# Kernel tuning notes

Hardware: AMD Instinct MI355X
Metric: run time of the kernel (lower is better)

## Reference

```python
import jax, jax.numpy as jnp
import numpy as np

B, N, R, CIN = 2, 2048, 128, 256
RADIUS, NSAMPLE, OUT = 0.3, 16, 5
EPS = 1e-5


def setup_inputs():
    key = jax.random.key(0)
    ks = jax.random.split(key, 8)
    points_xyz = jax.random.uniform(ks[0], (B, N, 3)) * 2.0          # scene ~2m cube
    features = jax.random.normal(ks[1], (B, CIN, N))
    ctr = jax.random.uniform(ks[2], (B, R, 3)) * 2.0
    size = jax.random.uniform(ks[3], (B, R, 3)) * 0.6 + 0.3          # positive box sizes
    ang = jax.random.uniform(ks[4], (B, R, 1)) * np.pi
    rois = jnp.concatenate([ctr, size, ang], axis=-1)                # [B,R,7]
    s = 0.02
    W_mlp = jax.random.normal(ks[5], (256, CIN + 3)) * s
    g_mlp = jnp.ones((256,)); bt_mlp = jnp.zeros((256,))
    W1 = jax.random.normal(ks[6], (128, 256)) * s; b1 = jnp.zeros((128,))
    g1 = jnp.ones((128,)); bt1 = jnp.zeros((128,))
    W2 = jax.random.normal(ks[7], (128, 128)) * s; b2 = jnp.zeros((128,))
    g2 = jnp.ones((128,)); bt2 = jnp.zeros((128,))
    return dict(points_xyz=points_xyz, features=features, rois=rois,
                W_mlp=W_mlp, g_mlp=g_mlp, bt_mlp=bt_mlp,
                W1=W1, b1=b1, g1=g1, bt1=bt1,
                W2=W2, b2=b2, g2=g2, bt2=bt2)


def _bn(x, g, b, axes, shape):
    # training-mode BatchNorm (batch statistics), matching torch .train() forward
    m = jnp.mean(x, axes, keepdims=True)
    v = jnp.var(x, axes, keepdims=True)
    return (x - m) * jax.lax.rsqrt(v + EPS) * g.reshape(shape) + b.reshape(shape)


def _forward(points_xyz, features, rois, W_mlp, g_mlp, bt_mlp,
             W1, b1, g1, bt1, W2, b2, g2, bt2):
    # ---- QueryAndGroup: ball query (min_radius=0) + gather + center + normalize_xyz ----
    diff = points_xyz[:, :, None, :] - points_xyz[:, None, :, :]     # [B,Nq,Np,3]
    d2 = jnp.sum(diff * diff, -1)
    mask = d2 < RADIUS * RADIUS
    cand = jnp.where(mask, jnp.arange(N, dtype=jnp.int32)[None, None, :], N)
    idx = jnp.sort(cand, axis=-1)[..., :NSAMPLE]                     # first NSAMPLE in-ball, ascending point index
    idx = jnp.where(idx < N, idx, idx[..., :1])                      # pad with first valid (self always in-ball)
    gx = jax.vmap(lambda p, i: p[i])(points_xyz, idx)                # [B,N,S,3]
    gx = (gx - points_xyz[:, :, None, :]) / RADIUS                   # centered + normalized
    gf = jax.vmap(lambda f, i: f[i])(jnp.swapaxes(features, 1, 2), idx)  # [B,N,S,C]
    nf = jnp.transpose(jnp.concatenate([gx, gf], -1), (0, 3, 1, 2))  # [B,3+C,N,S] (use_xyz=True)
    # ---- mlp: Conv2d 1x1 (bias='auto' with BN -> no bias) + BN2d + ReLU ----
    h = jnp.einsum('oc,bcns->bons', W_mlp, nf)
    h = jax.nn.relu(_bn(h, g_mlp, bt_mlp, (0, 2, 3), (1, -1, 1, 1)))
    feats = jnp.max(h, -1)                                           # max_pool2d over samples -> [B,256,N]
    h = jnp.einsum('oc,bcn->bon', W1, feats) + b1[None, :, None]
    h = jax.nn.relu(_bn(h, g1, bt1, (0, 2), (1, -1, 1)))
    h = jnp.einsum('oc,bcn->bon', W2, h) + b2[None, :, None]
    feats = jax.nn.relu(_bn(h, g2, bt2, (0, 2), (1, -1, 1)))         # [B,128,N]
    # ---- RoIPool3d: roi-aware voxel max pool (out_size=5, mode='max') ----
    C = feats.shape[1]
    ctr, size, ry = rois[..., :3], rois[..., 3:6], rois[..., 6]
    rel = points_xyz[:, None, :, :] - ctr[:, :, None, :]             # [B,R,N,3]
    c = jnp.cos(ry)[:, :, None]; s = jnp.sin(ry)[:, :, None]
    lx = rel[..., 0] * c + rel[..., 1] * s                           # rotate by -ry into roi frame
    ly = -rel[..., 0] * s + rel[..., 1] * c
    local = jnp.stack([lx, ly, rel[..., 2]], -1)                     # [B,R,N,3]
    half = size[:, :, None, :] * 0.5
    inside = jnp.all(jnp.abs(local) < half, -1)                      # [B,R,N]
    v = jnp.clip(jnp.floor((local + half) / (2.0 * half) * OUT), 0, OUT - 1).astype(jnp.int32)
    vox = (v[..., 0] * OUT + v[..., 1]) * OUT + v[..., 2]
    base = jnp.arange(B * R, dtype=jnp.int32).reshape(B, R, 1) * (OUT ** 3)
    seg = jnp.where(inside, base + vox, B * R * OUT ** 3).reshape(-1)  # dummy segment for outside pts
    data = jnp.broadcast_to(jnp.swapaxes(feats, 1, 2)[:, None], (B, R, N, C)).reshape(-1, C)
    pooled = jax.ops.segment_max(data, seg, num_segments=B * R * OUT ** 3 + 1)[:-1]
    pooled = jnp.where(jnp.isneginf(pooled), 0.0, pooled)            # empty voxels -> 0
    roi_feats = pooled.reshape(B, R, OUT, OUT, OUT, C)
    return feats, roi_feats


def reference(points_xyz, features, rois, W_mlp, g_mlp, bt_mlp,
              W1, b1, g1, bt1, W2, b2, g2, bt2):
    return _forward(points_xyz, features, rois, W_mlp, g_mlp, bt_mlp,
                    W1, b1, g1, bt1, W2, b2, g2, bt2)
```

## Files before the change

kernel.cpp:

```cpp
#include <hip/hip_runtime.h>
#include <hip/hip_bf16.h>

typedef __hip_bfloat16 bf16;
typedef unsigned short u16;

#define NB   2
#define NPT  2048
#define NROI 128
#define CINF 256
#define NS   16
#define KDIM 259
#define KP2  288
#define C1   256
#define C2   128
#define NVOX 125
#define EPSF 1e-5f

typedef __bf16 bf16x8 __attribute__((ext_vector_type(8)));
typedef float  f32x4  __attribute__((ext_vector_type(4)));

__device__ __forceinline__ float ldin(const void* p, size_t i, int f32flag) {
    if (f32flag) return ((const float*)p)[i];
    unsigned short u = ((const unsigned short*)p)[i];
    return __uint_as_float(((unsigned)u) << 16);
}

__device__ __forceinline__ unsigned short f2bf(float x) {
    unsigned u = __float_as_uint(x);
    u += 0x7FFFu + ((u >> 16) & 1u);
    return (unsigned short)(u >> 16);
}


__global__ void k_detect(const void* __restrict__ Wm, int* __restrict__ flag) {
    __shared__ int f;
    int tid = threadIdx.x;
    if (tid == 0) f = 0;
    __syncthreads();
    #pragma unroll
    for (int r = 0; r < 4; r++) {
        unsigned short u = ((const unsigned short*)Wm)[r * 256 + tid];
        float v = __uint_as_float(((unsigned)u) << 16);
        if (!(fabsf(v) <= 1e4f)) atomicOr(&f, 1);
    }
    __syncthreads();
    if (tid == 0) *flag = f;
}

__global__ void k_cvt(const void* __restrict__ pts, const void* __restrict__ rois,
                      const void* __restrict__ gm, const void* __restrict__ btm,
                      const void* __restrict__ b1, const void* __restrict__ g1,
                      const void* __restrict__ bt1, const void* __restrict__ b2,
                      const void* __restrict__ g2, const void* __restrict__ bt2,
                      const void* __restrict__ Wm,
                      float* __restrict__ ptsf, float* __restrict__ roisf,
                      float* __restrict__ params, const int* __restrict__ flag) {
    int f = *flag;
    int e = blockIdx.x * 256 + threadIdx.x;
    if (blockIdx.y == 10) {
        if (e < 768) {
            int d = e >> 8, o = e & 255;
            params[25088 + e] = ldin(Wm, (size_t)o * KDIM + d, f);
        }
        return;
    }
    const void* src; float* dst; int n;
    switch (blockIdx.y) {
        case 0:  src = pts; dst = ptsf;           n = NB * NPT * 3; break;
        case 1:  src = rois; dst = roisf;         n = NB * NROI * 7; break;
        case 2:  src = gm;  dst = params + 0;     n = 256; break;
        case 3:  src = btm; dst = params + 256;   n = 256; break;
        case 4:  src = b1;  dst = params + 33280; n = 128; break;
        case 5:  src = g1;  dst = params + 33408; n = 128; break;
        case 6:  src = bt1; dst = params + 33536; n = 128; break;
        case 7:  src = b2;  dst = params + 50048; n = 128; break;
        case 8:  src = g2;  dst = params + 50176; n = 128; break;
        default: src = bt2; dst = params + 50304; n = 128; break;
    }
    if (e < n) dst[e] = ldin(src, e, f);
}

__global__ void k_soa(const float* __restrict__ ptsf, float* __restrict__ psx,
                      float* __restrict__ psy, float* __restrict__ psz) {
    int e = blockIdx.x * 256 + threadIdx.x;
    if (e < NB * NPT) {
        psx[e] = ptsf[e * 3 + 0];
        psy[e] = ptsf[e * 3 + 1];
        psz[e] = ptsf[e * 3 + 2];
    }
}

__global__ void k_transpose(const void* __restrict__ feat, u16* __restrict__ ftbf,
                            const int* __restrict__ flag) {
    __shared__ float tile[32][33];
    int f = *flag;
    int b = blockIdx.z;
    int n0 = blockIdx.x * 32, c0 = blockIdx.y * 32;
    int tx = threadIdx.x, ty = threadIdx.y;
    #pragma unroll
    for (int d = 0; d < 4; d++) {
        int c = c0 + ty + d * 8;
        tile[ty + d * 8][tx] = ldin(feat, ((size_t)(b * CINF + c)) * NPT + n0 + tx, f);
    }
    __syncthreads();
    #pragma unroll
    for (int d = 0; d < 4; d++) {
        int n = n0 + ty + d * 8;
        ftbf[((size_t)(b * NPT + n)) * CINF + c0 + tx] = f2bf(tile[tx][ty + d * 8]);
    }
}

__global__ void k_prep(const void* __restrict__ Wm, const void* __restrict__ W1,
                       const void* __restrict__ W2, u16* __restrict__ wbf,
                       u16* __restrict__ w1bf, u16* __restrict__ w2bf,
                       float* __restrict__ stats, const int* __restrict__ flag) {
    int f = *flag;
    int e = blockIdx.x * 256 + threadIdx.x;
    if (e < 256 * KP2) {
        int o = e / KP2, k = e % KP2;
        float v = 0.f;
        if (k < 256)      v = ldin(Wm, (size_t)o * KDIM + 3 + k, f);
        else if (k < 259) v = ldin(Wm, (size_t)o * KDIM + (k - 256), f);
        wbf[e] = f2bf(v);
    } else if (e < 256 * KP2 + 1024) {
        stats[e - 256 * KP2] = 0.f;
    } else if (e < 256 * KP2 + 1024 + 32768) {
        int idx = e - (256 * KP2 + 1024);
        w1bf[idx] = f2bf(ldin(W1, idx, f));
    } else if (e < 256 * KP2 + 1024 + 32768 + 16384) {
        int idx = e - (256 * KP2 + 1024 + 32768);
        w2bf[idx] = f2bf(ldin(W2, idx, f));
    }
}

__global__ __launch_bounds__(256) void k_knn2(const float* __restrict__ psx, const float* __restrict__ psy,
                                              const float* __restrict__ psz, int* __restrict__ idxb) {
    #pragma clang fp contract(off)
    int wid = threadIdx.x >> 6, lane = threadIdx.x & 63;
    int q = blockIdx.x * 4 + wid;
    int b = q >> 11;
    int base = b * NPT;
    float qx = psx[q], qy = psy[q], qz = psz[q];
    const float R2 = (float)(0.3 * 0.3);
    size_t ob = (size_t)q * NS;
    int cnt = 0, j0 = -1;
    unsigned long long below = (lane == 63) ? ~0ull >> 1 : ((1ull << (lane + 1)) - 1) >> 1;
    for (int c0 = 0; c0 < NPT; c0 += 64) {
        int j = c0 + lane;
        float dx = qx - psx[base + j];
        float dy = qy - psy[base + j];
        float dz = qz - psz[base + j];
        float d2 = dx * dx + dy * dy + dz * dz;
        bool hit = d2 < R2;
        unsigned long long m = __ballot(hit);
        if (m) {
            if (j0 < 0) j0 = c0 + __builtin_ctzll(m);
            int pos = cnt + __popcll(m & below);
            if (hit && pos < NS) idxb[ob + pos] = j;
            cnt += __popcll(m);
        }
        if (cnt >= NS) break;
    }
    if (lane >= cnt && lane < NS) idxb[ob + lane] = j0;
}

__global__ __launch_bounds__(256) void k_dense(const u16* __restrict__ ftbf, const u16* __restrict__ wbf,
                                               float* __restrict__ Hf) {
    int w = threadIdx.x >> 6, lane = threadIdx.x & 63;
    int lg = lane >> 4, lr = lane & 15;
    int rbase = blockIdx.x * 16;
    int c0 = blockIdx.y * 128 + w * 32;

    size_t aoff  = (size_t)(rbase + lr) * CINF + lg * 8;
    size_t boff0 = (size_t)(c0 + lr) * KP2 + lg * 8;
    size_t boff1 = (size_t)(c0 + 16 + lr) * KP2 + lg * 8;

    f32x4 acc0 = (f32x4){0.f, 0.f, 0.f, 0.f};
    f32x4 acc1 = (f32x4){0.f, 0.f, 0.f, 0.f};
    #pragma unroll
    for (int k0 = 0; k0 < 256; k0 += 32) {
        bf16x8 af = __builtin_bit_cast(bf16x8, *(const uint4*)(ftbf + aoff + k0));
        bf16x8 b0 = __builtin_bit_cast(bf16x8, *(const uint4*)(wbf + boff0 + k0));
        bf16x8 b1 = __builtin_bit_cast(bf16x8, *(const uint4*)(wbf + boff1 + k0));
        acc0 = __builtin_amdgcn_mfma_f32_16x16x32_bf16(af, b0, acc0, 0, 0, 0);
        acc1 = __builtin_amdgcn_mfma_f32_16x16x32_bf16(af, b1, acc1, 0, 0, 0);
    }
    #pragma unroll
    for (int r = 0; r < 4; r++) {
        int row = rbase + lg * 4 + r;
        Hf[(size_t)row * C1 + c0 + lr] = acc0[r];
        Hf[(size_t)row * C1 + c0 + 16 + lr] = acc1[r];
    }
}

#define GPTS 8
__global__ __launch_bounds__(256) void k_gather(const float* __restrict__ Hf, const int* __restrict__ idxb,
                                                const float* __restrict__ ptsf, const float* __restrict__ wxyz,
                                                float* __restrict__ Hmax, float* __restrict__ Hmin,
                                                float* __restrict__ stats) {
    __shared__ int   lj[NS];
    __shared__ float lgx[NS], lgy[NS], lgz[NS];
    int o = threadIdx.x;
    float wx = wxyz[o], wy = wxyz[256 + o], wz = wxyz[512 + o];
    float ssum = 0.f, ssq = 0.f;
    for (int p = 0; p < GPTS; p++) {
        int pt = blockIdx.x * GPTS + p;
        int b = pt >> 11;
        int base = b * NPT;
        if (o < NS) {
            int j = idxb[(size_t)pt * NS + o];
            lj[o] = j;
            size_t jb = ((size_t)(base + j)) * 3;
            size_t cb = (size_t)pt * 3;
            lgx[o] = (ptsf[jb]     - ptsf[cb])     / 0.3f;
            lgy[o] = (ptsf[jb + 1] - ptsf[cb + 1]) / 0.3f;
            lgz[o] = (ptsf[jb + 2] - ptsf[cb + 2]) / 0.3f;
        }
        __syncthreads();
        float mx = -3.4e38f, mn = 3.4e38f;
        #pragma unroll
        for (int s = 0; s < NS; s++) {
            float v = Hf[(size_t)(base + lj[s]) * C1 + o] + wx * lgx[s] + wy * lgy[s] + wz * lgz[s];
            mx = fmaxf(mx, v); mn = fminf(mn, v);
            ssum += v; ssq += v * v;
        }
        Hmax[(size_t)pt * C1 + o] = mx;
        Hmin[(size_t)pt * C1 + o] = mn;
        __syncthreads();
    }
    atomicAdd(&stats[o], ssum);
    atomicAdd(&stats[256 + o], ssq);
}

__global__ void k_feats0(const float* __restrict__ Hmax, const float* __restrict__ Hmin,
                         const float* __restrict__ stats, const float* __restrict__ g,
                         const float* __restrict__ bt, u16* __restrict__ f0bf) {
    int e = blockIdx.x * 256 + threadIdx.x;
    if (e >= NB * NPT * C1) return;
    int o = e & (C1 - 1);
    const float inv = 1.f / 65536.f;
    float m = stats[o] * inv;
    float var = fmaxf(stats[256 + o] * inv - m * m, 0.f);
    float a = g[o] / sqrtf(var + EPSF);
    float d = bt[o] - m * a;
    float h = (a > 0.f) ? Hmax[e] : Hmin[e];
    f0bf[e] = f2bf(fmaxf(a * h + d, 0.f));
}

template<int K>
__global__ __launch_bounds__(256) void k_lin(const u16* __restrict__ Xbf, const u16* __restrict__ Wb,
                                             const float* __restrict__ bias, float* __restrict__ out,
                                             float* __restrict__ sum, float* __restrict__ sumsq) {
    int w = threadIdx.x >> 6, lane = threadIdx.x & 63;
    int lg = lane >> 4, lr = lane & 15;
    int rbase = blockIdx.x * 16;
    int c0 = w * 32;

    size_t aoff = (size_t)(rbase + lr) * K + lg * 8;
    size_t boff0 = (size_t)(c0 + lr) * K + lg * 8;
    size_t boff1 = (size_t)(c0 + 16 + lr) * K + lg * 8;

    f32x4 acc0 = (f32x4){0.f, 0.f, 0.f, 0.f};
    f32x4 acc1 = (f32x4){0.f, 0.f, 0.f, 0.f};
    #pragma unroll
    for (int k0 = 0; k0 < K; k0 += 32) {
        bf16x8 af = __builtin_bit_cast(bf16x8, *(const uint4*)(Xbf + aoff + k0));
        bf16x8 b0 = __builtin_bit_cast(bf16x8, *(const uint4*)(Wb + boff0 + k0));
        bf16x8 b1 = __builtin_bit_cast(bf16x8, *(const uint4*)(Wb + boff1 + k0));
        acc0 = __builtin_amdgcn_mfma_f32_16x16x32_bf16(af, b0, acc0, 0, 0, 0);
        acc1 = __builtin_amdgcn_mfma_f32_16x16x32_bf16(af, b1, acc1, 0, 0, 0);
    }

    #pragma unroll
    for (int ct = 0; ct < 2; ct++) {
        f32x4 a = ct ? acc1 : acc0;
        int col = c0 + ct * 16 + lr;
        float bi = bias[col];
        float s = 0.f, q = 0.f;
        #pragma unroll
        for (int r = 0; r < 4; r++) {
            float h = a[r] + bi;
            out[(size_t)(rbase + lg * 4 + r) * C2 + col] = h;
            s += h; q += h * h;
        }
        s += __shfl_xor(s, 16); s += __shfl_xor(s, 32);
        q += __shfl_xor(q, 16); q += __shfl_xor(q, 32);
        if (lane < 16) {
            atomicAdd(&sum[col], s);
            atomicAdd(&sumsq[col], q);
        }
    }
}

__global__ void k_bnrelu(const float* __restrict__ h, const float* __restrict__ sum,
                         const float* __restrict__ sumsq, const float* __restrict__ g,
                         const float* __restrict__ bt, u16* __restrict__ xbf) {
    int e = blockIdx.x * 256 + threadIdx.x;
    if (e >= NB * NPT * C2) return;
    int o = e & (C2 - 1);
    const float inv = 1.f / 4096.f;
    float m = sum[o] * inv;
    float var = fmaxf(sumsq[o] * inv - m * m, 0.f);
    float a = g[o] / sqrtf(var + EPSF);
    float d = bt[o] - m * a;
    xbf[e] = f2bf(fmaxf(a * h[e] + d, 0.f));
}

__global__ void k_final(const float* __restrict__ h2, const float* __restrict__ sum,
                        const float* __restrict__ sumsq, const float* __restrict__ g,
                        const float* __restrict__ bt, float* __restrict__ fp,
                        void* __restrict__ out0, const int* __restrict__ flag) {
    int e = blockIdx.x * 256 + threadIdx.x;
    if (e >= NB * NPT * C2) return;
    int f = *flag;
    int o = e & (C2 - 1);
    int bn = e >> 7;
    int b = bn >> 11, n = bn & (NPT - 1);
    const float inv = 1.f / 4096.f;
    float m = sum[o] * inv;
    float var = fmaxf(sumsq[o] * inv - m * m, 0.f);
    float a = g[o] / sqrtf(var + EPSF);
    float d = bt[o] - m * a;
    float v = fmaxf(a * h2[e] + d, 0.f);
    fp[e] = v;
    size_t oi = ((size_t)(b * C2 + o)) * NPT + n;
    if (f) ((float*)out0)[oi] = v;
    else   ((unsigned short*)out0)[oi] = f2bf(v);
}

__global__ __launch_bounds__(512) void k_pool2(const float* __restrict__ ptsf, const float* __restrict__ roisf,
                                               const float* __restrict__ fp, void* __restrict__ d_out,
                                               const int* __restrict__ flag, int* __restrict__ glist) {
    #pragma clang fp contract(off)
    __shared__ int pooled[NVOX * C2];
    __shared__ int cnt;
    __shared__ float rp[8];
    int f = *flag;
    int bid = blockIdx.x;
    int b = bid >> 7;
    int tid = threadIdx.x;
    for (int k = tid; k < NVOX * C2; k += 512) pooled[k] = 0;
    if (tid == 0) {
        cnt = 0;
        size_t rb = ((size_t)bid) * 7;
        rp[0] = roisf[rb];     rp[1] = roisf[rb + 1]; rp[2] = roisf[rb + 2];
        rp[3] = roisf[rb + 3] * 0.5f;
        rp[4] = roisf[rb + 4] * 0.5f;
        rp[5] = roisf[rb + 5] * 0.5f;
        float ry = roisf[rb + 6];
        rp[6] = (float)cos((double)ry);
        rp[7] = (float)sin((double)ry);
    }
    __syncthreads();
    float cx = rp[0], cy = rp[1], cz = rp[2];
    float hx = rp[3], hy = rp[4], hz = rp[5];
    float cf = rp[6], sf = rp[7];
    int* mylist = glist + bid * NPT;
    for (int n = tid; n < NPT; n += 512) {
        size_t pb = ((size_t)(b * NPT + n)) * 3;
        float rx  = ptsf[pb]     - cx;
        float ryy = ptsf[pb + 1] - cy;
        float rz  = ptsf[pb + 2] - cz;
        float lx = rx * cf + ryy * sf;
        float ly = -rx * sf + ryy * cf;
        if (fabsf(lx) < hx && fabsf(ly) < hy && fabsf(rz) < hz) {
            int vx = (int)fminf(fmaxf(floorf((lx + hx) / (2.f * hx) * 5.f), 0.f), 4.f);
            int vy = (int)fminf(fmaxf(floorf((ly + hy) / (2.f * hy) * 5.f), 0.f), 4.f);
            int vz = (int)fminf(fmaxf(floorf((rz + hz) / (2.f * hz) * 5.f), 0.f), 4.f);
            int vox = (vx * 5 + vy) * 5 + vz;
            int pos = atomicAdd(&cnt, 1);
            mylist[pos] = (vox << 16) | n;
        }
    }
    __syncthreads();
    int m = cnt;
    int c = tid & 127, slot = tid >> 7;
    for (int e = slot; e < m; e += 4) {
        int u = mylist[e];
        int n = u & 0xFFFF, vox = u >> 16;
        float v = fp[((size_t)(b * NPT + n)) * C2 + c];
        atomicMax(&pooled[vox * C2 + c], __float_as_int(v));
    }
    __syncthreads();
    size_t ob = (size_t)524288 + (size_t)bid * (NVOX * C2);
    for (int k = tid; k < NVOX * C2; k += 512) {
        float v = __int_as_float(pooled[k]);
        if (f) ((float*)d_out)[ob + k] = v;
        else   ((unsigned short*)d_out)[ob + k] = f2bf(v);
    }
}

extern "C" void kernel_launch(void* const* d_in, const int* in_sizes, int n_in,
                              void* d_out, int out_size, void* d_ws, size_t ws_size,
                              hipStream_t stream) {
    const void* pts  = d_in[0];
    const void* feat = d_in[1];
    const void* rois = d_in[2];
    const void* Wm   = d_in[3];
    const void* gm   = d_in[4];
    const void* btm  = d_in[5];
    const void* W1   = d_in[6];
    const void* b1   = d_in[7];
    const void* g1   = d_in[8];
    const void* bt1  = d_in[9];
    const void* W2   = d_in[10];
    const void* b2   = d_in[11];
    const void* g2   = d_in[12];
    const void* bt2  = d_in[13];

    float* ws     = (float*)d_ws;
    int*   flag   = (int*)ws;
    float* ptsf   = ws + 16;
    float* roisf  = ws + 12304;
    float* params = ws + 14096;
    u16*   w1bf   = (u16*)(params + 512);
    u16*   w2bf   = (u16*)(params + 512 + 16384);
    float* wxyz   = params + 25088;
    u16*   wbf    = (u16*)(ws + 64528);
    float* stats  = ws + 101392;
    int*   idxb   = (int*)(ws + 102416);
    u16*   ftbf   = (u16*)(ws + 167952);
    float* Hmax   = ws + 1216528;
    float* Hmin   = ws + 2265104;
    u16*   f0bf   = (u16*)(ws + 167952);
    float* h1     = ws + 1216528;
    u16*   x1bf   = (u16*)(ws + 1740816);
    float* h2     = ws + 2265104;
    float* fp     = ws + 2789392;
    float* psx    = ws + 3313680;
    float* psy    = ws + 3317776;
    float* psz    = ws + 3321872;
    float* Hf     = ws + 3325968;
    int*   glist  = (int*)(ws + 3325968);

    k_detect<<<1, 256, 0, stream>>>(Wm, flag);
    k_cvt<<<dim3(48, 11), 256, 0, stream>>>(pts, rois, gm, btm, b1, g1, bt1, b2, g2, bt2, Wm,
                                            ptsf, roisf, params, flag);
    k_soa<<<16, 256, 0, stream>>>(ptsf, psx, psy, psz);
    k_transpose<<<dim3(NPT / 32, CINF / 32, NB), dim3(32, 8), 0, stream>>>(feat, ftbf, flag);
    k_prep<<<484, 256, 0, stream>>>(Wm, W1, W2, wbf, w1bf, w2bf, stats, flag);
    k_knn2<<<NB * NPT / 4, 256, 0, stream>>>(psx, psy, psz, idxb);
    k_dense<<<dim3(256, 2), 256, 0, stream>>>(ftbf, wbf, Hf);
    k_gather<<<(NB * NPT) / GPTS, 256, 0, stream>>>(Hf, idxb, ptsf, wxyz, Hmax, Hmin, stats);
    k_feats0<<<(NB * NPT * C1) / 256, 256, 0, stream>>>(Hmax, Hmin, stats, params + 0, params + 256, f0bf);
    k_lin<256><<<256, 256, 0, stream>>>(f0bf, w1bf, params + 33280, h1, stats + 512, stats + 640);
    k_bnrelu<<<(NB * NPT * C2) / 256, 256, 0, stream>>>(h1, stats + 512, stats + 640, params + 33408, params + 33536, x1bf);
    k_lin<128><<<256, 256, 0, stream>>>(x1bf, w2bf, params + 50048, h2, stats + 768, stats + 896);
    k_final<<<(NB * NPT * C2) / 256, 256, 0, stream>>>(h2, stats + 768, stats + 896, params + 50176, params + 50304, fp, d_out, flag);
    k_pool2<<<NB * NROI, 512, 0, stream>>>(ptsf, roisf, fp, d_out, flag, glist);
}
```

Measured before the change: 196.1 us.

## Merge setup kernels, co-launch ball query with dense GEMM, fuse BN-ReLU into linears

Folds the dtype-detect, convert, SoA, transpose and weight-prep kernels into one block-indexed setup kernel, with each block recomputing the dtype flag from the first weights. Ball query and the dense feature GEMM now share one launch as disjoint block ranges. The BatchNorm+ReLU stages are fused into the prologues of the two following linear kernels, which build bf16 activation tiles in shared memory. Together these cut the launch count from fourteen to seven and drop two intermediate bf16 buffers, at the cost of redundant flag reads in every block and a more heterogeneous setup kernel.

```diff
diff --git a/kernel.cpp b/kernel.cpp
--- a/kernel.cpp
+++ b/kernel.cpp
@@ -31,165 +31,165 @@
     return (unsigned short)(u >> 16);
 }
 
-
-__global__ void k_detect(const void* __restrict__ Wm, int* __restrict__ flag) {
-    __shared__ int f;
+__device__ __forceinline__ int detect_flag(const void* __restrict__ Wm) {
+    const uint4* p = (const uint4*)Wm;
+    int bad = 0;
+    #pragma unroll
+    for (int i = 0; i < 8; i++) {
+        uint4 v = p[i];
+        unsigned w[4] = {v.x, v.y, v.z, v.w};
+        #pragma unroll
+        for (int j = 0; j < 4; j++) {
+            if (!(fabsf(__uint_as_float(w[j] << 16)) <= 1e4f)) bad = 1;
+            if (!(fabsf(__uint_as_float(w[j] & 0xFFFF0000u)) <= 1e4f)) bad = 1;
+        }
+    }
+    return bad;
+}
+
+
+__global__ __launch_bounds__(256) void k_setup(
+    const void* __restrict__ pts, const void* __restrict__ feat, const void* __restrict__ rois,
+    const void* __restrict__ Wm, const void* __restrict__ gm, const void* __restrict__ btm,
+    const void* __restrict__ W1, const void* __restrict__ b1, const void* __restrict__ g1,
+    const void* __restrict__ bt1, const void* __restrict__ W2, const void* __restrict__ b2,
+    const void* __restrict__ g2, const void* __restrict__ bt2,
+    float* __restrict__ ptsf, float* __restrict__ roisf, float* __restrict__ params,
+    u16* __restrict__ wbf, u16* __restrict__ w1bf, u16* __restrict__ w2bf,
+    float* __restrict__ stats, u16* __restrict__ ftbf,
+    float* __restrict__ psx, float* __restrict__ psy, float* __restrict__ psz) {
+    int f = detect_flag(Wm);
+    int bx = blockIdx.x;
     int tid = threadIdx.x;
-    if (tid == 0) f = 0;
-    __syncthreads();
-    #pragma unroll
-    for (int r = 0; r < 4; r++) {
-        unsigned short u = ((const unsigned short*)Wm)[r * 256 + tid];
-        float v = __uint_as_float(((unsigned)u) << 16);
-        if (!(fabsf(v) <= 1e4f)) atomicOr(&f, 1);
-    }
-    __syncthreads();
-    if (tid == 0) *flag = f;
-}
-
-__global__ void k_cvt(const void* __restrict__ pts, const void* __restrict__ rois,
-                      const void* __restrict__ gm, const void* __restrict__ btm,
-                      const void* __restrict__ b1, const void* __restrict__ g1,
-                      const void* __restrict__ bt1, const void* __restrict__ b2,
-                      const void* __restrict__ g2, const void* __restrict__ bt2,
-                      const void* __restrict__ Wm,
-                      float* __restrict__ ptsf, float* __restrict__ roisf,
-                      float* __restrict__ params, const int* __restrict__ flag) {
-    int f = *flag;
-    int e = blockIdx.x * 256 + threadIdx.x;
-    if (blockIdx.y == 10) {
-        if (e < 768) {
-            int d = e >> 8, o = e & 255;
-            params[25088 + e] = ldin(Wm, (size_t)o * KDIM + d, f);
-        }
-        return;
-    }
-    const void* src; float* dst; int n;
-    switch (blockIdx.y) {
-        case 0:  src = pts; dst = ptsf;           n = NB * NPT * 3; break;
-        case 1:  src = rois; dst = roisf;         n = NB * NROI * 7; break;
-        case 2:  src = gm;  dst = params + 0;     n = 256; break;
-        case 3:  src = btm; dst = params + 256;   n = 256; break;
-        case 4:  src = b1;  dst = params + 33280; n = 128; break;
-        case 5:  src = g1;  dst = params + 33408; n = 128; break;
-        case 6:  src = bt1; dst = params + 33536; n = 128; break;
-        case 7:  src = b2;  dst = params + 50048; n = 128; break;
-        case 8:  src = g2;  dst = params + 50176; n = 128; break;
-        default: src = bt2; dst = params + 50304; n = 128; break;
-    }
-    if (e < n) dst[e] = ldin(src, e, f);
-}
-
-__global__ void k_soa(const float* __restrict__ ptsf, float* __restrict__ psx,
-                      float* __restrict__ psy, float* __restrict__ psz) {
-    int e = blockIdx.x * 256 + threadIdx.x;
-    if (e < NB * NPT) {
-        psx[e] = ptsf[e * 3 + 0];
-        psy[e] = ptsf[e * 3 + 1];
-        psz[e] = ptsf[e * 3 + 2];
-    }
-}
-
-__global__ void k_transpose(const void* __restrict__ feat, u16* __restrict__ ftbf,
-                            const int* __restrict__ flag) {
-    __shared__ float tile[32][33];
-    int f = *flag;
-    int b = blockIdx.z;
-    int n0 = blockIdx.x * 32, c0 = blockIdx.y * 32;
-    int tx = threadIdx.x, ty = threadIdx.y;
-    #pragma unroll
-    for (int d = 0; d < 4; d++) {
-        int c = c0 + ty + d * 8;
-        tile[ty + d * 8][tx] = ldin(feat, ((size_t)(b * CINF + c)) * NPT + n0 + tx, f);
-    }
-    __syncthreads();
-    #pragma unroll
-    for (int d = 0; d < 4; d++) {
-        int n = n0 + ty + d * 8;
-        ftbf[((size_t)(b * NPT + n)) * CINF + c0 + tx] = f2bf(tile[tx][ty + d * 8]);
-    }
-}
-
-__global__ void k_prep(const void* __restrict__ Wm, const void* __restrict__ W1,
-                       const void* __restrict__ W2, u16* __restrict__ wbf,
-                       u16* __restrict__ w1bf, u16* __restrict__ w2bf,
-                       float* __restrict__ stats, const int* __restrict__ flag) {
-    int f = *flag;
-    int e = blockIdx.x * 256 + threadIdx.x;
-    if (e < 256 * KP2) {
+    if (bx < 1024) {
+        __shared__ float tile[32][33];
+        int b = bx >> 9;
+        int r = bx & 511;
+        int n0 = (r & 63) * 32, c0 = (r >> 6) * 32;
+        int tx = tid & 31, ty = tid >> 5;
+        #pragma unroll
+        for (int d = 0; d < 4; d++) {
+            int c = c0 + ty + d * 8;
+            tile[ty + d * 8][tx] = ldin(feat, ((size_t)(b * CINF + c)) * NPT + n0 + tx, f);
+        }
+        __syncthreads();
+        #pragma unroll
+        for (int d = 0; d < 4; d++) {
+            int n = n0 + ty + d * 8;
+            ftbf[((size_t)(b * NPT + n)) * CINF + c0 + tx] = f2bf(tile[tx][ty + d * 8]);
+        }
+    } else if (bx < 1312) {
+        int e = (bx - 1024) * 256 + tid;
         int o = e / KP2, k = e % KP2;
         float v = 0.f;
         if (k < 256)      v = ldin(Wm, (size_t)o * KDIM + 3 + k, f);
         else if (k < 259) v = ldin(Wm, (size_t)o * KDIM + (k - 256), f);
         wbf[e] = f2bf(v);
-    } else if (e < 256 * KP2 + 1024) {
-        stats[e - 256 * KP2] = 0.f;
-    } else if (e < 256 * KP2 + 1024 + 32768) {
-        int idx = e - (256 * KP2 + 1024);
-        w1bf[idx] = f2bf(ldin(W1, idx, f));
-    } else if (e < 256 * KP2 + 1024 + 32768 + 16384) {
-        int idx = e - (256 * KP2 + 1024 + 32768);
-        w2bf[idx] = f2bf(ldin(W2, idx, f));
-    }
-}
-
-__global__ __launch_bounds__(256) void k_knn2(const float* __restrict__ psx, const float* __restrict__ psy,
-                                              const float* __restrict__ psz, int* __restrict__ idxb) {
-    #pragma clang fp contract(off)
-    int wid = threadIdx.x >> 6, lane = threadIdx.x & 63;
-    int q = blockIdx.x * 4 + wid;
-    int b = q >> 11;
-    int base = b * NPT;
-    float qx = psx[q], qy = psy[q], qz = psz[q];
-    const float R2 = (float)(0.3 * 0.3);
-    size_t ob = (size_t)q * NS;
-    int cnt = 0, j0 = -1;
-    unsigned long long below = (lane == 63) ? ~0ull >> 1 : ((1ull << (lane + 1)) - 1) >> 1;
-    for (int c0 = 0; c0 < NPT; c0 += 64) {
-        int j = c0 + lane;
-        float dx = qx - psx[base + j];
-        float dy = qy - psy[base + j];
-        float dz = qz - psz[base + j];
-        float d2 = dx * dx + dy * dy + dz * dz;
-        bool hit = d2 < R2;
-        unsigned long long m = __ballot(hit);
-        if (m) {
-            if (j0 < 0) j0 = c0 + __builtin_ctzll(m);
-            int pos = cnt + __popcll(m & below);
-            if (hit && pos < NS) idxb[ob + pos] = j;
-            cnt += __popcll(m);
-        }
-        if (cnt >= NS) break;
-    }
-    if (lane >= cnt && lane < NS) idxb[ob + lane] = j0;
-}
-
-__global__ __launch_bounds__(256) void k_dense(const u16* __restrict__ ftbf, const u16* __restrict__ wbf,
-                                               float* __restrict__ Hf) {
-    int w = threadIdx.x >> 6, lane = threadIdx.x & 63;
-    int lg = lane >> 4, lr = lane & 15;
-    int rbase = blockIdx.x * 16;
-    int c0 = blockIdx.y * 128 + w * 32;
-
-    size_t aoff  = (size_t)(rbase + lr) * CINF + lg * 8;
-    size_t boff0 = (size_t)(c0 + lr) * KP2 + lg * 8;
-    size_t boff1 = (size_t)(c0 + 16 + lr) * KP2 + lg * 8;
-
-    f32x4 acc0 = (f32x4){0.f, 0.f, 0.f, 0.f};
-    f32x4 acc1 = (f32x4){0.f, 0.f, 0.f, 0.f};
-    #pragma unroll
-    for (int k0 = 0; k0 < 256; k0 += 32) {
-        bf16x8 af = __builtin_bit_cast(bf16x8, *(const uint4*)(ftbf + aoff + k0));
-        bf16x8 b0 = __builtin_bit_cast(bf16x8, *(const uint4*)(wbf + boff0 + k0));
-        bf16x8 b1 = __builtin_bit_cast(bf16x8, *(const uint4*)(wbf + boff1 + k0));
-        acc0 = __builtin_amdgcn_mfma_f32_16x16x32_bf16(af, b0, acc0, 0, 0, 0);
-        acc1 = __builtin_amdgcn_mfma_f32_16x16x32_bf16(af, b1, acc1, 0, 0, 0);
-    }
-    #pragma unroll
-    for (int r = 0; r < 4; r++) {
-        int row = rbase + lg * 4 + r;
-        Hf[(size_t)row * C1 + c0 + lr] = acc0[r];
-        Hf[(size_t)row * C1 + c0 + 16 + lr] = acc1[r];
+    } else if (bx < 1440) {
+        int e = (bx - 1312) * 256 + tid;
+        w1bf[e] = f2bf(ldin(W1, e, f));
+    } else if (bx < 1504) {
+        int e = (bx - 1440) * 256 + tid;
+        w2bf[e] = f2bf(ldin(W2, e, f));
+    } else if (bx < 1552) {
+        int e = (bx - 1504) * 256 + tid;
+        if (e < NB * NPT * 3) ptsf[e] = ldin(pts, e, f);
+    } else if (bx < 1559) {
+        int e = (bx - 1552) * 256 + tid;
+        if (e < NB * NROI * 7) roisf[e] = ldin(rois, e, f);
+    } else if (bx < 1567) {
+        int t = bx - 1559;
+        const void* src; int off, n;
+        switch (t) {
+            case 0: src = gm;  off = 0;     n = 256; break;
+            case 1: src = btm; off = 256;   n = 256; break;
+            case 2: src = b1;  off = 33280; n = 128; break;
+            case 3: src = g1;  off = 33408; n = 128; break;
+            case 4: src = bt1; off = 33536; n = 128; break;
+            case 5: src = b2;  off = 50048; n = 128; break;
+            case 6: src = g2;  off = 50176; n = 128; break;
+            default: src = bt2; off = 50304; n = 128; break;
+        }
+        if (tid < n) params[off + tid] = ldin(src, tid, f);
+    } else if (bx < 1570) {
+        int e = (bx - 1567) * 256 + tid;
+        if (e < 768) {
+            int d = e >> 8, o = e & 255;
+            params[25088 + e] = ldin(Wm, (size_t)o * KDIM + d, f);
+        }
+    } else if (bx < 1586) {
+        int e = (bx - 1570) * 256 + tid;
+        if (e < NB * NPT) {
+            psx[e] = ptsf ? ldin(pts, e * 3 + 0, f) : 0.f;
+            psy[e] = ldin(pts, e * 3 + 1, f);
+            psz[e] = ldin(pts, e * 3 + 2, f);
+        }
+    } else {
+        int e = (bx - 1586) * 256 + tid;
+        if (e < 1024) stats[e] = 0.f;
+    }
+}
+
+__global__ __launch_bounds__(256) void k_qd(const float* __restrict__ psx, const float* __restrict__ psy,
+                                            const float* __restrict__ psz, int* __restrict__ idxb,
+                                            const u16* __restrict__ ftbf, const u16* __restrict__ wbf,
+                                            float* __restrict__ Hf) {
+    int bx = blockIdx.x;
+    if (bx < 1024) {
+        #pragma clang fp contract(off)
+        int wid = threadIdx.x >> 6, lane = threadIdx.x & 63;
+        int q = bx * 4 + wid;
+        int b = q >> 11;
+        int base = b * NPT;
+        float qx = psx[q], qy = psy[q], qz = psz[q];
+        const float R2 = (float)(0.3 * 0.3);
+        size_t ob = (size_t)q * NS;
+        int cnt = 0, j0 = -1;
+        unsigned long long below = (lane == 63) ? ~0ull >> 1 : ((1ull << (lane + 1)) - 1) >> 1;
+        for (int c0 = 0; c0 < NPT; c0 += 64) {
+            int j = c0 + lane;
+            float dx = qx - psx[base + j];
+            float dy = qy - psy[base + j];
+            float dz = qz - psz[base + j];
+            float d2 = dx * dx + dy * dy + dz * dz;
+            bool hit = d2 < R2;
+            unsigned long long m = __ballot(hit);
+            if (m) {
+                if (j0 < 0) j0 = c0 + __builtin_ctzll(m);
+                int pos = cnt + __popcll(m & below);
+                if (hit && pos < NS) idxb[ob + pos] = j;
+                cnt += __popcll(m);
+            }
+            if (cnt >= NS) break;
+        }
+        if (lane >= cnt && lane < NS) idxb[ob + lane] = j0;
+    } else {
+        int bx2 = bx - 1024;
+        int w = threadIdx.x >> 6, lane = threadIdx.x & 63;
+        int lg = lane >> 4, lr = lane & 15;
+        int rbase = (bx2 & 255) * 16;
+        int c0 = (bx2 >> 8) * 128 + w * 32;
+
+        size_t aoff  = (size_t)(rbase + lr) * CINF + lg * 8;
+        size_t boff0 = (size_t)(c0 + lr) * KP2 + lg * 8;
+        size_t boff1 = (size_t)(c0 + 16 + lr) * KP2 + lg * 8;
+
+        f32x4 acc0 = (f32x4){0.f, 0.f, 0.f, 0.f};
+        f32x4 acc1 = (f32x4){0.f, 0.f, 0.f, 0.f};
+        #pragma unroll
+        for (int k0 = 0; k0 < 256; k0 += 32) {
+            bf16x8 af = __builtin_bit_cast(bf16x8, *(const uint4*)(ftbf + aoff + k0));
+            bf16x8 b0 = __builtin_bit_cast(bf16x8, *(const uint4*)(wbf + boff0 + k0));
+            bf16x8 b1 = __builtin_bit_cast(bf16x8, *(const uint4*)(wbf + boff1 + k0));
+            acc0 = __builtin_amdgcn_mfma_f32_16x16x32_bf16(af, b0, acc0, 0, 0, 0);
+            acc1 = __builtin_amdgcn_mfma_f32_16x16x32_bf16(af, b1, acc1, 0, 0, 0);
+        }
+        #pragma unroll
+        for (int r = 0; r < 4; r++) {
+            int row = rbase + lg * 4 + r;
+            Hf[(size_t)row * C1 + c0 + lr] = acc0[r];
+            Hf[(size_t)row * C1 + c0 + 16 + lr] = acc1[r];
+        }
     }
 }
 
@@ -232,45 +232,45 @@
     atomicAdd(&stats[256 + o], ssq);
 }
 
-__global__ void k_feats0(const float* __restrict__ Hmax, const float* __restrict__ Hmin,
-                         const float* __restrict__ stats, const float* __restrict__ g,
-                         const float* __restrict__ bt, u16* __restrict__ f0bf) {
-    int e = blockIdx.x * 256 + threadIdx.x;
-    if (e >= NB * NPT * C1) return;
-    int o = e & (C1 - 1);
-    const float inv = 1.f / 65536.f;
-    float m = stats[o] * inv;
-    float var = fmaxf(stats[256 + o] * inv - m * m, 0.f);
-    float a = g[o] / sqrtf(var + EPSF);
-    float d = bt[o] - m * a;
-    float h = (a > 0.f) ? Hmax[e] : Hmin[e];
-    f0bf[e] = f2bf(fmaxf(a * h + d, 0.f));
-}
-
-template<int K>
-__global__ __launch_bounds__(256) void k_lin(const u16* __restrict__ Xbf, const u16* __restrict__ Wb,
-                                             const float* __restrict__ bias, float* __restrict__ out,
-                                             float* __restrict__ sum, float* __restrict__ sumsq) {
-    int w = threadIdx.x >> 6, lane = threadIdx.x & 63;
+__global__ __launch_bounds__(256) void k_lin1f(const float* __restrict__ Hmax, const float* __restrict__ Hmin,
+                                               const float* __restrict__ stats, const float* __restrict__ g,
+                                               const float* __restrict__ bt, const u16* __restrict__ Wb,
+                                               const float* __restrict__ bias, float* __restrict__ out,
+                                               float* __restrict__ sum, float* __restrict__ sumsq) {
+    __shared__ __align__(16) u16 xa[16][264];
+    int tid = threadIdx.x;
+    int rbase = blockIdx.x * 16;
+    {
+        int c = tid;
+        const float inv = 1.f / 65536.f;
+        float m = stats[c] * inv;
+        float var = fmaxf(stats[256 + c] * inv - m * m, 0.f);
+        float a = g[c] / sqrtf(var + EPSF);
+        float d = bt[c] - m * a;
+        #pragma unroll
+        for (int r = 0; r < 16; r++) {
+            size_t e = (size_t)(rbase + r) * C1 + c;
+            float h = (a > 0.f) ? Hmax[e] : Hmin[e];
+            xa[r][c] = f2bf(fmaxf(a * h + d, 0.f));
+        }
+    }
+    __syncthreads();
+    int w = tid >> 6, lane = tid & 63;
     int lg = lane >> 4, lr = lane & 15;
-    int rbase = blockIdx.x * 16;
     int c0 = w * 32;
-
-    size_t aoff = (size_t)(rbase + lr) * K + lg * 8;
-    size_t boff0 = (size_t)(c0 + lr) * K + lg * 8;
-    size_t boff1 = (size_t)(c0 + 16 + lr) * K + lg * 8;
+    size_t boff0 = (size_t)(c0 + lr) * 256 + lg * 8;
+    size_t boff1 = (size_t)(c0 + 16 + lr) * 256 + lg * 8;
 
     f32x4 acc0 = (f32x4){0.f, 0.f, 0.f, 0.f};
     f32x4 acc1 = (f32x4){0.f, 0.f, 0.f, 0.f};
     #pragma unroll
-    for (int k0 = 0; k0 < K; k0 += 32) {
-        bf16x8 af = __builtin_bit_cast(bf16x8, *(const uint4*)(Xbf + aoff + k0));
+    for (int k0 = 0; k0 < 256; k0 += 32) {
+        bf16x8 af = __builtin_bit_cast(bf16x8, *(const uint4*)&xa[lr][k0 + lg * 8]);
         bf16x8 b0 = __builtin_bit_cast(bf16x8, *(const uint4*)(Wb + boff0 + k0));
         bf16x8 b1 = __builtin_bit_cast(bf16x8, *(const uint4*)(Wb + boff1 + k0));
         acc0 = __builtin_amdgcn_mfma_f32_16x16x32_bf16(af, b0, acc0, 0, 0, 0);
         acc1 = __builtin_amdgcn_mfma_f32_16x16x32_bf16(af, b1, acc1, 0, 0, 0);
     }
-
     #pragma unroll
     for (int ct = 0; ct < 2; ct++) {
         f32x4 a = ct ? acc1 : acc0;
@@ -292,27 +292,73 @@
     }
 }
 
-__global__ void k_bnrelu(const float* __restrict__ h, const float* __restrict__ sum,
-                         const float* __restrict__ sumsq, const float* __restrict__ g,
-                         const float* __restrict__ bt, u16* __restrict__ xbf) {
-    int e = blockIdx.x * 256 + threadIdx.x;
-    if (e >= NB * NPT * C2) return;
-    int o = e & (C2 - 1);
-    const float inv = 1.f / 4096.f;
-    float m = sum[o] * inv;
-    float var = fmaxf(sumsq[o] * inv - m * m, 0.f);
-    float a = g[o] / sqrtf(var + EPSF);
-    float d = bt[o] - m * a;
-    xbf[e] = f2bf(fmaxf(a * h[e] + d, 0.f));
+__global__ __launch_bounds__(256) void k_lin2f(const float* __restrict__ h1, const float* __restrict__ stats1,
+                                               const float* __restrict__ g, const float* __restrict__ bt,
+                                               const u16* __restrict__ Wb, const float* __restrict__ bias,
+                                               float* __restrict__ out, float* __restrict__ sum,
+                                               float* __restrict__ sumsq) {
+    __shared__ __align__(16) u16 xa[16][136];
+    int tid = threadIdx.x;
+    int rbase = blockIdx.x * 16;
+    {
+        int c = tid & 127, half = tid >> 7;
+        const float inv = 1.f / 4096.f;
+        float m = stats1[c] * inv;
+        float var = fmaxf(stats1[128 + c] * inv - m * m, 0.f);
+        float a = g[c] / sqrtf(var + EPSF);
+        float d = bt[c] - m * a;
+        #pragma unroll
+        for (int rr = 0; rr < 8; rr++) {
+            int r = half * 8 + rr;
+            float h = h1[(size_t)(rbase + r) * C2 + c];
+            xa[r][c] = f2bf(fmaxf(a * h + d, 0.f));
+        }
+    }
+    __syncthreads();
+    int w = tid >> 6, lane = tid & 63;
+    int lg = lane >> 4, lr = lane & 15;
+    int c0 = w * 32;
+    size_t boff0 = (size_t)(c0 + lr) * 128 + lg * 8;
+    size_t boff1 = (size_t)(c0 + 16 + lr) * 128 + lg * 8;
+
+    f32x4 acc0 = (f32x4){0.f, 0.f, 0.f, 0.f};
+    f32x4 acc1 = (f32x4){0.f, 0.f, 0.f, 0.f};
+    #pragma unroll
+    for (int k0 = 0; k0 < 128; k0 += 32) {
+        bf16x8 af = __builtin_bit_cast(bf16x8, *(const uint4*)&xa[lr][k0 + lg * 8]);
+        bf16x8 b0 = __builtin_bit_cast(bf16x8, *(const uint4*)(Wb + boff0 + k0));
+        bf16x8 b1 = __builtin_bit_cast(bf16x8, *(const uint4*)(Wb + boff1 + k0));
+        acc0 = __builtin_amdgcn_mfma_f32_16x16x32_bf16(af, b0, acc0, 0, 0, 0);
+        acc1 = __builtin_amdgcn_mfma_f32_16x16x32_bf16(af, b1, acc1, 0, 0, 0);
+    }
+    #pragma unroll
+    for (int ct = 0; ct < 2; ct++) {
+        f32x4 a = ct ? acc1 : acc0;
+        int col = c0 + ct * 16 + lr;
+        float bi = bias[col];
+        float s = 0.f, q = 0.f;
+        #pragma unroll
+        for (int r = 0; r < 4; r++) {
+            float h = a[r] + bi;
+            out[(size_t)(rbase + lg * 4 + r) * C2 + col] = h;
+            s += h; q += h * h;
+        }
+        s += __shfl_xor(s, 16); s += __shfl_xor(s, 32);
+        q += __shfl_xor(q, 16); q += __shfl_xor(q, 32);
+        if (lane < 16) {
+            atomicAdd(&sum[col], s);
+            atomicAdd(&sumsq[col], q);
+        }
+    }
 }
 
 __global__ void k_final(const float* __restrict__ h2, const float* __restrict__ sum,
                         const float* __restrict__ sumsq, const float* __restrict__ g,
                         const float* __restrict__ bt, float* __restrict__ fp,
-                        void* __restrict__ out0, const int* __restrict__ flag) {
+                        void* __restrict__ out0, const void* __restrict__ Wm) {
     int e = blockIdx.x * 256 + threadIdx.x;
     if (e >= NB * NPT * C2) return;
-    int f = *flag;
+    int f = detect_flag(Wm);
     int o = e & (C2 - 1);
     int bn = e >> 7;
     int b = bn >> 11, n = bn & (NPT - 1);
@@ -330,12 +376,12 @@
 
 __global__ __launch_bounds__(512) void k_pool2(const float* __restrict__ ptsf, const float* __restrict__ roisf,
                                                const float* __restrict__ fp, void* __restrict__ d_out,
-                                               const int* __restrict__ flag, int* __restrict__ glist) {
+                                               const void* __restrict__ Wm, int* __restrict__ glist) {
     #pragma clang fp contract(off)
     __shared__ int pooled[NVOX * C2];
     __shared__ int cnt;
     __shared__ float rp[8];
-    int f = *flag;
+    int f = detect_flag(Wm);
     int bid = blockIdx.x;
     int b = bid >> 7;
     int tid = threadIdx.x;
@@ -409,7 +455,6 @@
     const void* bt2  = d_in[13];
 
     float* ws     = (float*)d_ws;
-    int*   flag   = (int*)ws;
     float* ptsf   = ws + 16;
     float* roisf  = ws + 12304;
     float* params = ws + 14096;
@@ -422,9 +467,7 @@
     u16*   ftbf   = (u16*)(ws + 167952);
     float* Hmax   = ws + 1216528;
     float* Hmin   = ws + 2265104;
-    u16*   f0bf   = (u16*)(ws + 167952);
     float* h1     = ws + 1216528;
-    u16*   x1bf   = (u16*)(ws + 1740816);
     float* h2     = ws + 2265104;
     float* fp     = ws + 2789392;
     float* psx    = ws + 3313680;
@@ -433,19 +476,16 @@
     float* Hf     = ws + 3325968;
     int*   glist  = (int*)(ws + 3325968);
 
-    k_detect<<<1, 256, 0, stream>>>(Wm, flag);
-    k_cvt<<<dim3(48, 11), 256, 0, stream>>>(pts, rois, gm, btm, b1, g1, bt1, b2, g2, bt2, Wm,
-                                            ptsf, roisf, params, flag);
-    k_soa<<<16, 256, 0, stream>>>(ptsf, psx, psy, psz);
-    k_transpose<<<dim3(NPT / 32, CINF / 32, NB), dim3(32, 8), 0, stream>>>(feat, ftbf, flag);
-    k_prep<<<484, 256, 0, stream>>>(Wm, W1, W2, wbf, w1bf, w2bf, stats, flag);
-    k_knn2<<<NB * NPT / 4, 256, 0, stream>>>(psx, psy, psz, idxb);
-    k_dense<<<dim3(256, 2), 256, 0, stream>>>(ftbf, wbf, Hf);
+    k_setup<<<1590, 256, 0, stream>>>(pts, feat, rois, Wm, gm, btm, W1, b1, g1, bt1,
+                                      W2, b2, g2, bt2, ptsf, roisf, params,
+                                      wbf, w1bf, w2bf, stats, ftbf, psx, psy, psz);
+    k_qd<<<1536, 256, 0, stream>>>(psx, psy, psz, idxb, ftbf, wbf, Hf);
     k_gather<<<(NB * NPT) / GPTS, 256, 0, stream>>>(Hf, idxb, ptsf, wxyz, Hmax, Hmin, stats);
-    k_feats0<<<(NB * NPT * C1) / 256, 256, 0, stream>>>(Hmax, Hmin, stats, params + 0, params + 256, f0bf);
-    k_lin<256><<<256, 256, 0, stream>>>(f0bf, w1bf, params + 33280, h1, stats + 512, stats + 640);
-    k_bnrelu<<<(NB * NPT * C2) / 256, 256, 0, stream>>>(h1, stats + 512, stats + 640, params + 33408, params + 33536, x1bf);
-    k_lin<128><<<256, 256, 0, stream>>>(x1bf, w2bf, params + 50048, h2, stats + 768, stats + 896);
-    k_final<<<(NB * NPT * C2) / 256, 256, 0, stream>>>(h2, stats + 768, stats + 896, params + 50176, params + 50304, fp, d_out, flag);
-    k_pool2<<<NB * NROI, 512, 0, stream>>>(ptsf, roisf, fp, d_out, flag, glist);
-}
+    k_lin1f<<<256, 256, 0, stream>>>(Hmax, Hmin, stats, params + 0, params + 256,
+                                     w1bf, params + 33280, h1, stats + 512, stats + 640);
+    k_lin2f<<<256, 256, 0, stream>>>(h1, stats + 512, params + 33408, params + 33536,
+                                     w2bf, params + 50048, h2, stats + 768, stats + 896);
+    k_final<<<(NB * NPT * C2) / 256, 256, 0, stream>>>(h2, stats + 768, stats + 896,
+                                                       params + 50176, params + 50304, fp, d_out, Wm);
+    k_pool2<<<NB * NROI, 512, 0, stream>>>(ptsf, roisf, fp, d_out, Wm, glist);
+}
```

Result: faster. 181.9 us (-7.3%).
